# Kernel optimization log

Measured on AMD Instinct MI355X. Metric: run time of the kernel, lower is better.

Reference implementation:

```python
import jax, jax.numpy as jnp
import numpy as np

EPS = 1e-7
MIN_NORM = 1e-15
PROJ_EPS = 4e-3
C = 1.0
HEADS = 4
NEG_SLOPE = 0.2

def artanh(x):
    x = jnp.clip(x, -1.0 + EPS, 1.0 - EPS)
    return 0.5 * (jnp.log1p(x) - jnp.log1p(-x))

def _norm(x):
    return jnp.clip(jnp.linalg.norm(x, axis=-1, keepdims=True), MIN_NORM)

def proj(x, c):
    n = _norm(x)
    maxnorm = (1.0 - PROJ_EPS) / jnp.sqrt(c)
    return jnp.where(n > maxnorm, x / n * maxnorm, x)

def expmap0(u, c):
    sc = jnp.sqrt(c)
    n = _norm(u)
    return jnp.tanh(sc * n) * u / (sc * n)

def logmap0(p, c):
    sc = jnp.sqrt(c)
    n = _norm(p)
    return artanh(sc * n) * p / (sc * n)

def mobius_add(x, y, c):
    x2 = jnp.sum(x * x, -1, keepdims=True)
    y2 = jnp.sum(y * y, -1, keepdims=True)
    xy = jnp.sum(x * y, -1, keepdims=True)
    num = (1 + 2 * c * xy + c * y2) * x + (1 - c * x2) * y
    den = 1 + 2 * c * xy + c * c * x2 * y2
    return num / jnp.clip(den, MIN_NORM)

def mobius_matvec(m, x, c):
    sc = jnp.sqrt(c)
    xn = _norm(x)
    mx = x @ m.T
    mxn = _norm(mx)
    res = jnp.tanh(mxn / xn * artanh(sc * xn)) * mx / (mxn * sc)
    zero = jnp.all(mx == 0, axis=-1, keepdims=True)
    return jnp.where(zero, 0.0, res)

def segment_softmax(scores, seg, n):
    # scores: [E, H], seg: [E] destination node ids
    smax = jax.ops.segment_max(scores, seg, num_segments=n)
    smax = jnp.where(jnp.isfinite(smax), smax, 0.0)
    ex = jnp.exp(scores - smax[seg])
    den = jax.ops.segment_sum(ex, seg, num_segments=n)
    return ex / jnp.clip(den[seg], MIN_NORM)


def setup_inputs() -> dict:
    key = jax.random.key(0)
    ks = jax.random.split(key, 6)
    N, D_IN, D_OUT, E = 50000, 128, 128, 800000
    x = 0.01 * jax.random.normal(ks[0], (N, D_IN), dtype=jnp.float32)
    W = (math := np.sqrt(2.0 * 6.0 / (D_IN + D_OUT))) * jax.random.uniform(ks[1], (D_OUT, D_IN), dtype=jnp.float32, minval=-1.0, maxval=1.0)
    lin_bias = jnp.zeros((D_OUT,), jnp.float32)
    att = 0.1 * jax.random.normal(ks[2], (1, HEADS, 2 * (D_OUT // HEADS)), dtype=jnp.float32)
    conv_bias = jnp.zeros((D_OUT,), jnp.float32)
    src = jax.random.randint(ks[3], (E,), 0, N, dtype=jnp.int32)
    # guarantee no self loops (module removes them before adding canonical ones)
    dst = (src + 1 + jax.random.randint(ks[4], (E,), 0, N - 1, dtype=jnp.int32)) % N
    return {"x": x, "W": W, "lin_bias": lin_bias, "att": att,
            "conv_bias": conv_bias, "edge_src": src, "edge_dst": dst}


def reference(x, W, lin_bias, att, conv_bias, edge_src, edge_dst):
    N = x.shape[0]
    H = HEADS
    # ---- HypLinear (c=1, eval mode so no dropout) ----
    h = proj(mobius_matvec(W, x, C), C)
    hyp_bias = proj(expmap0(lin_bias, C), C)   # proj_tan0 is identity on Poincare ball
    h = proj(mobius_add(h, hyp_bias, C), C)
    D = h.shape[-1] // H
    # ---- add self loops ----
    loops = jnp.arange(N, dtype=edge_src.dtype)
    src = jnp.concatenate([edge_src, loops])   # j (source)
    dst = jnp.concatenate([edge_dst, loops])   # i (target / aggregation index)
    # ---- tangent-space GAT message passing ----
    log_x = logmap0(h, C).reshape(N, H, D)
    x_i = log_x[dst]                            # [E, H, D]
    x_j = log_x[src]                            # [E, H, D]
    att_i, att_j = att[0, :, :D], att[0, :, D:]
    alpha = jnp.einsum('ehd,hd->eh', x_i, att_i) + jnp.einsum('ehd,hd->eh', x_j, att_j)
    alpha = jax.nn.leaky_relu(alpha, NEG_SLOPE)
    alpha = segment_softmax(alpha, dst, N)      # [E, H]
    msg = x_j * alpha[:, :, None]
    out = jax.ops.segment_sum(msg, dst, num_segments=N)  # [N, H, D]
    out = out.reshape(N, H * D) + conv_bias
    # ---- update / activation / map back to manifold ----
    out = jax.nn.relu(out)                      # proj_tan0 is identity
    return proj(expmap0(out, C), C)
```

## Files before the change

kernel.cpp:

```cpp
#include <hip/hip_runtime.h>
#include <hip/hip_fp16.h>
#include <math.h>

#define EPSF 1e-7f
#define MIN_NORM 1e-15f
#define MAXNORM 0.996f
#define NEG_SLOPE 0.2f

typedef __attribute__((ext_vector_type(8))) short short8;
typedef __attribute__((ext_vector_type(4))) float f32x4;

__device__ __forceinline__ float wave_reduce_sum(float v) {
    #pragma unroll
    for (int m = 1; m < 64; m <<= 1) v += __shfl_xor(v, m, 64);
    return v;
}

__device__ __forceinline__ float artanhf_(float x) {
    x = fminf(fmaxf(x, -1.f + EPSF), 1.f - EPSF);
    return 0.5f * (log1pf(x) - log1pf(-x));
}

__device__ __forceinline__ float lrelu(float a) {
    return a < 0.f ? a * NEG_SLOPE : a;
}

__device__ __forceinline__ unsigned short f2bf(float f) {
    unsigned u = __float_as_uint(f);
    u += 0x7FFFu + ((u >> 16) & 1u);
    return (unsigned short)(u >> 16);
}
__device__ __forceinline__ float bf2f(unsigned short h) {
    return __uint_as_float(((unsigned)h) << 16);
}

__global__ void prep_kernel(const float* __restrict__ W,
                            unsigned short* __restrict__ whi,
                            unsigned short* __restrict__ wlo,
                            const float* __restrict__ lin_bias,
                            float* __restrict__ bbuf) {
    if (blockIdx.x == 64) {
        if (threadIdx.x >= 64) return;
        int lane = threadIdx.x;
        float u0 = lin_bias[lane], u1 = lin_bias[lane + 64];
        float n2 = wave_reduce_sum(u0 * u0 + u1 * u1);
        float n = fmaxf(sqrtf(n2), MIN_NORM);
        float s = tanhf(n) / n;
        float b0 = s * u0, b1 = s * u1;
        float bn = fmaxf(tanhf(n), MIN_NORM);
        float fn2 = bn * bn;
        if (bn > MAXNORM) { float f = MAXNORM / bn; b0 *= f; b1 *= f; fn2 = MAXNORM * MAXNORM; }
        bbuf[lane] = b0;
        bbuf[lane + 64] = b1;
        if (lane == 0) bbuf[128] = fn2;
        return;
    }
    int idx = blockIdx.x * 256 + threadIdx.x;
    int i = idx & 7, l = (idx >> 3) & 63, ts = idx >> 9;
    int s = ts & 3, t = ts >> 2;
    int o = t * 16 + (l & 15);
    int k = s * 32 + ((l >> 4) * 8) + i;
    float f = W[o * 128 + k];
    unsigned short h = f2bf(f);
    unsigned short lo = f2bf(f - bf2f(h));
    whi[idx] = h;
    wlo[idx] = lo;
}

#define DPAD 132
__global__ __launch_bounds__(256) void node_kernel(
    const float* __restrict__ x,
    const unsigned short* __restrict__ whi, const unsigned short* __restrict__ wlo,
    const float* __restrict__ bbuf, const float* __restrict__ att,
    unsigned short* __restrict__ log_xb,
    float* __restrict__ s_i, float* __restrict__ s_j, int N)
{
    __shared__ float mxs[16][DPAD];
    __shared__ float xn2s[16];
    int tid = threadIdx.x, wave = tid >> 6, lane = tid & 63;
    int nbase = blockIdx.x * 16;
    int arow = lane & 15, kgrp = lane >> 4;
    int anode = min(nbase + arow, N - 1);

    f32x4 acc0 = {0.f, 0.f, 0.f, 0.f};
    f32x4 acc1 = {0.f, 0.f, 0.f, 0.f};
    int t0 = wave * 2, t1 = wave * 2 + 1;
    float x2loc = 0.f;

    #pragma unroll
    for (int s = 0; s < 4; ++s) {
        const float* xp = x + (size_t)anode * 128 + s * 32 + kgrp * 8;
        float4 xa = *(const float4*)xp;
        float4 xb = *(const float4*)(xp + 4);
        float xv[8] = {xa.x, xa.y, xa.z, xa.w, xb.x, xb.y, xb.z, xb.w};
        short8 ahi, alo;
        #pragma unroll
        for (int i = 0; i < 8; ++i) {
            unsigned short h = f2bf(xv[i]);
            unsigned short l = f2bf(xv[i] - bf2f(h));
            ahi[i] = (short)h;
            alo[i] = (short)l;
        }
        if (wave == 0) {
            #pragma unroll
            for (int i = 0; i < 8; ++i) x2loc = fmaf(xv[i], xv[i], x2loc);
        }
        short8 bh0 = *(const short8*)(whi + ((size_t)(t0 * 4 + s) * 64 + lane) * 8);
        short8 bl0 = *(const short8*)(wlo + ((size_t)(t0 * 4 + s) * 64 + lane) * 8);
        short8 bh1 = *(const short8*)(whi + ((size_t)(t1 * 4 + s) * 64 + lane) * 8);
        short8 bl1 = *(const short8*)(wlo + ((size_t)(t1 * 4 + s) * 64 + lane) * 8);
        acc0 = __builtin_amdgcn_mfma_f32_16x16x32_bf16(ahi, bh0, acc0, 0, 0, 0);
        acc0 = __builtin_amdgcn_mfma_f32_16x16x32_bf16(alo, bh0, acc0, 0, 0, 0);
        acc0 = __builtin_amdgcn_mfma_f32_16x16x32_bf16(ahi, bl0, acc0, 0, 0, 0);
        acc1 = __builtin_amdgcn_mfma_f32_16x16x32_bf16(ahi, bh1, acc1, 0, 0, 0);
        acc1 = __builtin_amdgcn_mfma_f32_16x16x32_bf16(alo, bh1, acc1, 0, 0, 0);
        acc1 = __builtin_amdgcn_mfma_f32_16x16x32_bf16(ahi, bl1, acc1, 0, 0, 0);
    }
    if (wave == 0) {
        x2loc += __shfl_xor(x2loc, 16, 64);
        x2loc += __shfl_xor(x2loc, 32, 64);
        if (lane < 16) xn2s[lane] = x2loc;
    }
    #pragma unroll
    for (int r = 0; r < 4; ++r) {
        mxs[kgrp * 4 + r][t0 * 16 + arow] = acc0[r];
        mxs[kgrp * 4 + r][t1 * 16 + arow] = acc1[r];
    }
    __syncthreads();

    int g16 = lane >> 4, l16 = lane & 15;
    int nn = wave * 4 + g16;
    int node = nbase + nn;
    bool valid = node < N;
    int head = l16 >> 2;
    int dbase = l16 * 8;
    int dd8 = (l16 & 3) * 8;
    float bb[8], aiv[8], ajv[8];
    #pragma unroll
    for (int j = 0; j < 8; ++j) {
        bb[j] = bbuf[dbase + j];
        aiv[j] = att[head * 64 + dd8 + j];
        ajv[j] = att[head * 64 + 32 + dd8 + j];
    }
    float y2 = bbuf[128];

    float4 va = *(const float4*)&mxs[nn][dbase];
    float4 vb = *(const float4*)&mxs[nn][dbase + 4];
    float v[8] = {va.x, va.y, va.z, va.w, vb.x, vb.y, vb.z, vb.w};

    float mq = 0.f;
    #pragma unroll
    for (int j = 0; j < 8; ++j) mq = fmaf(v[j], v[j], mq);
    #pragma unroll
    for (int m = 1; m < 16; m <<= 1) mq += __shfl_xor(mq, m, 64);

    float xn2 = xn2s[nn];
    float xn = fmaxf(sqrtf(xn2), MIN_NORM);
    float mxn = fmaxf(sqrtf(mq), MIN_NORM);
    float t = tanhf(mxn / xn * artanhf_(xn));
    float scl = t / mxn;
    bool zero = (mq == 0.f);
    float r[8];
    #pragma unroll
    for (int j = 0; j < 8; ++j) r[j] = zero ? 0.f : scl * v[j];
    float rn2 = zero ? 0.f : t * t;
    float rn = zero ? MIN_NORM : fmaxf(fabsf(t), MIN_NORM);
    float x2 = rn2;
    if (rn > MAXNORM) {
        float f = MAXNORM / rn;
        #pragma unroll
        for (int j = 0; j < 8; ++j) r[j] *= f;
        x2 = MAXNORM * MAXNORM;
    }
    float xy = 0.f;
    #pragma unroll
    for (int j = 0; j < 8; ++j) xy = fmaf(r[j], bb[j], xy);
    #pragma unroll
    for (int m = 1; m < 16; m <<= 1) xy += __shfl_xor(xy, m, 64);
    float cA = 1.f + 2.f * xy + y2;
    float cB = 1.f - x2;
    float dn = fmaxf(1.f + 2.f * xy + x2 * y2, MIN_NORM);
    float inv = 1.f / dn;
    float h[8];
    #pragma unroll
    for (int j = 0; j < 8; ++j) h[j] = (cA * r[j] + cB * bb[j]) * inv;
    float hq = 0.f;
    #pragma unroll
    for (int j = 0; j < 8; ++j) hq = fmaf(h[j], h[j], hq);
    #pragma unroll
    for (int m = 1; m < 16; m <<= 1) hq += __shfl_xor(hq, m, 64);
    float hn = fmaxf(sqrtf(hq), MIN_NORM);
    float ln2 = hq;
    if (hn > MAXNORM) {
        float f = MAXNORM / hn;
        #pragma unroll
        for (int j = 0; j < 8; ++j) h[j] *= f;
        ln2 = MAXNORM * MAXNORM;
    }
    float lnn = fmaxf(sqrtf(ln2), MIN_NORM);
    float ls = artanhf_(lnn) / lnn;
    float lv[8];
    #pragma unroll
    for (int j = 0; j < 8; ++j) lv[j] = ls * h[j];

    if (valid) {
        uint4 pk;
        pk.x = (unsigned)f2bf(lv[0]) | ((unsigned)f2bf(lv[1]) << 16);
        pk.y = (unsigned)f2bf(lv[2]) | ((unsigned)f2bf(lv[3]) << 16);
        pk.z = (unsigned)f2bf(lv[4]) | ((unsigned)f2bf(lv[5]) << 16);
        pk.w = (unsigned)f2bf(lv[6]) | ((unsigned)f2bf(lv[7]) << 16);
        *(uint4*)&log_xb[(size_t)node * 128 + dbase] = pk;
    }
    float pi = 0.f, pj = 0.f;
    #pragma unroll
    for (int j = 0; j < 8; ++j) {
        pi = fmaf(lv[j], aiv[j], pi);
        pj = fmaf(lv[j], ajv[j], pj);
    }
    pi += __shfl_xor(pi, 1, 64); pi += __shfl_xor(pi, 2, 64);
    pj += __shfl_xor(pj, 1, 64); pj += __shfl_xor(pj, 2, 64);
    if (valid && (l16 & 3) == 0) {
        int pos = ((head & 1) << 1) | (head >> 1);
        s_i[(size_t)node * 4 + pos] = pi;
        s_j[(size_t)node * 4 + pos] = pj;
    }
}

__global__ void buildw_kernel(const int* __restrict__ src, const int* __restrict__ dst,
                              int E, const float* __restrict__ s_i,
                              const float* __restrict__ s_j,
                              int* __restrict__ head, int4* __restrict__ pair16)
{
    int e = blockIdx.x * blockDim.x + threadIdx.x;
    if (e >= E) return;
    int s_ = src[e], d_ = dst[e];
    int prev = atomicExch(&head[(size_t)d_ * 16 + (e & 15)], e);
    float4 si = *(const float4*)(s_i + (size_t)d_ * 4);
    float4 sj = *(const float4*)(s_j + (size_t)s_ * 4);
    float w0 = __expf(lrelu(si.x + sj.x));
    float w1 = __expf(lrelu(si.y + sj.y));
    float w2 = __expf(lrelu(si.z + sj.z));
    float w3 = __expf(lrelu(si.w + sj.w));
    __half2 h01 = __floats2half2_rn(w0, w1);
    __half2 h23 = __floats2half2_rn(w2, w3);
    int4 pr;
    pr.x = s_ << 8;
    pr.y = prev;
    pr.z = *(int*)&h01;
    pr.w = *(int*)&h23;
    pair16[e] = pr;
}

#define MAXS 128
__global__ __launch_bounds__(256) void aggregate_kernel(
    const int* __restrict__ head, const int4* __restrict__ pair16,
    const float* __restrict__ s_i, const float* __restrict__ s_j,
    const unsigned short* __restrict__ log_xb, const float* __restrict__ conv_bias,
    float* __restrict__ out, int N)
{
    __shared__ __align__(16) int slist[4][MAXS];
    __shared__ __align__(16) unsigned wlist[4][MAXS * 2];
    __shared__ int scnt[4];
    int tid = threadIdx.x, wave = tid >> 6, lane = tid & 63;
    int n = blockIdx.x * 4 + wave;
    bool valid = n < N;

    if (lane == 0) scnt[wave] = 0;
    __syncthreads();

    int resume = -1;
    if (valid && lane < 16) {
        int e = head[(size_t)n * 16 + lane];
        while (e >= 0) {
            int4 pr = pair16[e];
            int pos = atomicAdd(&scnt[wave], 1);
            if (pos < MAXS) {
                slist[wave][pos] = pr.x;
                wlist[wave][pos * 2]     = (unsigned)pr.z;
                wlist[wave][pos * 2 + 1] = (unsigned)pr.w;
                e = pr.y;
            } else { resume = e; break; }
        }
    }
    __syncthreads();

    int g = lane >> 5;
    float acc0 = 0.f, acc1 = 0.f, dna = 0.f, dnb = 0.f;

    int deg = 0;
    if (valid) {
        deg = min(scnt[wave], MAXS);
        float2 si2  = *(const float2*)(s_i + (size_t)n * 4 + g * 2);
        float2 sj2n = *(const float2*)(s_j + (size_t)n * 4 + g * 2);
        float ea = __expf(lrelu(si2.x + sj2n.x));
        float eb = __expf(lrelu(si2.y + sj2n.y));
        dna = ea; dnb = eb;
        const unsigned short* mrow = log_xb + (size_t)n * 128;
        acc0 = ea * bf2f(mrow[lane]);
        acc1 = eb * bf2f(mrow[lane + 64]);

        const int* sl = slist[wave];
        const unsigned* wlv = wlist[wave];
        int i = 0;
        for (; i + 4 <= deg; i += 4) {
            int4 offq = *(const int4*)&sl[i];
            int offs[4] = {offq.x, offq.y, offq.z, offq.w};
            unsigned ww[4];
            unsigned short ma[4], mb[4];
            #pragma unroll
            for (int j = 0; j < 4; ++j) {
                ww[j] = wlv[(i + j) * 2 + g];
                const unsigned short* mr =
                    (const unsigned short*)((const char*)log_xb + offs[j]);
                ma[j] = mr[lane];
                mb[j] = mr[lane + 64];
            }
            #pragma unroll
            for (int j = 0; j < 4; ++j) {
                float2 wf = __half22float2(*(const __half2*)&ww[j]);
                dna += wf.x; dnb += wf.y;
                acc0 = fmaf(wf.x, bf2f(ma[j]), acc0);
                acc1 = fmaf(wf.y, bf2f(mb[j]), acc1);
            }
        }
        for (; i < deg; ++i) {
            unsigned w = wlv[i * 2 + g];
            const unsigned short* mr =
                (const unsigned short*)((const char*)log_xb + sl[i]);
            float2 wf = __half22float2(*(const __half2*)&w);
            dna += wf.x; dnb += wf.y;
            acc0 = fmaf(wf.x, bf2f(mr[lane]), acc0);
            acc1 = fmaf(wf.y, bf2f(mr[lane + 64]), acc1);
        }
    }

    unsigned long long mask = __ballot(resume >= 0);
    while (mask) {
        int l = __ffsll((long long)mask) - 1;
        int e = __shfl(resume, l, 64);
        while (e >= 0) {
            int off = 0, nx = -1, wz = 0, wwd = 0;
            if (lane == 0) { int4 pr = pair16[e]; off = pr.x; nx = pr.y; wz = pr.z; wwd = pr.w; }
            off = __shfl(off, 0, 64);
            wz = __shfl(wz, 0, 64);
            wwd = __shfl(wwd, 0, 64);
            e = __shfl(nx, 0, 64);
            unsigned wsel = (unsigned)(g ? wwd : wz);
            float2 wf = __half22float2(*(const __half2*)&wsel);
            const unsigned short* mr = (const unsigned short*)((const char*)log_xb + off);
            dna += wf.x; dnb += wf.y;
            acc0 = fmaf(wf.x, bf2f(mr[lane]), acc0);
            acc1 = fmaf(wf.y, bf2f(mr[lane + 64]), acc1);
        }
        mask &= mask - 1;
    }

    if (!valid) return;

    float v0 = acc0 / fmaxf(dna, MIN_NORM) + conv_bias[lane];
    float v1 = acc1 / fmaxf(dnb, MIN_NORM) + conv_bias[lane + 64];
    v0 = fmaxf(v0, 0.f);
    v1 = fmaxf(v1, 0.f);
    float n2 = wave_reduce_sum(v0 * v0 + v1 * v1);
    float nn = fmaxf(sqrtf(n2), MIN_NORM);
    float tv = tanhf(nn);
    float s = tv / nn;
    float r0 = s * v0, r1 = s * v1;
    float rn = fmaxf(tv, MIN_NORM);
    if (rn > MAXNORM) { float f = MAXNORM / rn; r0 *= f; r1 *= f; }
    out[(size_t)n * 128 + lane] = r0;
    out[(size_t)n * 128 + 64 + lane] = r1;
}

extern "C" void kernel_launch(void* const* d_in, const int* in_sizes, int n_in,
                              void* d_out, int out_size, void* d_ws, size_t ws_size,
                              hipStream_t stream)
{
    const float* x        = (const float*)d_in[0];
    const float* W        = (const float*)d_in[1];
    const float* lin_bias = (const float*)d_in[2];
    const float* att      = (const float*)d_in[3];
    const float* conv_bias= (const float*)d_in[4];
    const int*   esrc     = (const int*)d_in[5];
    const int*   edst     = (const int*)d_in[6];
    int N = in_sizes[0] / 128;
    int E = in_sizes[5];
    float* out = (float*)d_out;

    char* p = (char*)d_ws;
    float* bbuf   = (float*)p;  p += 256 * 4;
    unsigned short* whi = (unsigned short*)p; p += 16384 * 2;
    unsigned short* wlo = (unsigned short*)p; p += 16384 * 2;
    float* s_i    = (float*)p;  p += (size_t)N * 4 * 4;
    float* s_j    = (float*)p;  p += (size_t)N * 4 * 4;
    int*   head   = (int*)p;    p += (size_t)N * 16 * 4;
    int4*  pair16 = (int4*)p;   p += (size_t)E * 16;
    unsigned short* log_xb = (unsigned short*)p; p += (size_t)N * 128 * 2;

    hipMemsetAsync(head, 0xFF, (size_t)N * 16 * 4, stream);

    prep_kernel<<<65, 256, 0, stream>>>(W, whi, wlo, lin_bias, bbuf);
    int nTiles = (N + 15) / 16;
    node_kernel<<<nTiles, 256, 0, stream>>>(x, whi, wlo, bbuf, att, log_xb, s_i, s_j, N);
    buildw_kernel<<<(E + 255) / 256, 256, 0, stream>>>(esrc, edst, E, s_i, s_j, head, pair16);
    aggregate_kernel<<<(N + 3) / 4, 256, 0, stream>>>(
        head, pair16, s_i, s_j, log_xb, conv_bias, out, N);
}
```

Before: 130.3 us.

## Move edge attention weight computation into aggregation and slim edge list records

The edge build kernel now stores only (src, next) pairs, 8 bytes instead of 16, and runs before the node kernel because it no longer depends on attention scores. Attention exponentials are computed per edge inside the aggregation kernel's list walk from s_i/s_j, which removes one pass over edge data but adds a random s_j gather there. The aggregation inner loop gains an 8-way unrolled path, and tanh/artanh switch to fast exp/log intrinsics, which may lose a little accuracy near the clamp boundaries.

```diff
diff --git a/kernel.cpp b/kernel.cpp
--- a/kernel.cpp
+++ b/kernel.cpp
@@ -16,9 +16,14 @@
     return v;
 }
 
-__device__ __forceinline__ float artanhf_(float x) {
+__device__ __forceinline__ float fast_tanh(float x) {
+    float e = __expf(2.f * x);
+    return 1.f - 2.f / (e + 1.f);
+}
+
+__device__ __forceinline__ float fast_artanh(float x) {
     x = fminf(fmaxf(x, -1.f + EPSF), 1.f - EPSF);
-    return 0.5f * (log1pf(x) - log1pf(-x));
+    return 0.5f * __logf((1.f + x) / (1.f - x));
 }
 
 __device__ __forceinline__ float lrelu(float a) {
@@ -157,7 +162,7 @@
     float xn2 = xn2s[nn];
     float xn = fmaxf(sqrtf(xn2), MIN_NORM);
     float mxn = fmaxf(sqrtf(mq), MIN_NORM);
-    float t = tanhf(mxn / xn * artanhf_(xn));
+    float t = fast_tanh(mxn / xn * fast_artanh(xn));
     float scl = t / mxn;
     bool zero = (mq == 0.f);
     float r[8];
@@ -198,7 +203,7 @@
         ln2 = MAXNORM * MAXNORM;
     }
     float lnn = fmaxf(sqrtf(ln2), MIN_NORM);
-    float ls = artanhf_(lnn) / lnn;
+    float ls = fast_artanh(lnn) / lnn;
     float lv[8];
     #pragma unroll
     for (int j = 0; j < 8; ++j) lv[j] = ls * h[j];
@@ -226,34 +231,19 @@
     }
 }
 
-__global__ void buildw_kernel(const int* __restrict__ src, const int* __restrict__ dst,
-                              int E, const float* __restrict__ s_i,
-                              const float* __restrict__ s_j,
-                              int* __restrict__ head, int4* __restrict__ pair16)
+__global__ void build_kernel(const int* __restrict__ src, const int* __restrict__ dst,
+                             int E, int* __restrict__ head, int2* __restrict__ pair)
 {
     int e = blockIdx.x * blockDim.x + threadIdx.x;
     if (e >= E) return;
     int s_ = src[e], d_ = dst[e];
     int prev = atomicExch(&head[(size_t)d_ * 16 + (e & 15)], e);
-    float4 si = *(const float4*)(s_i + (size_t)d_ * 4);
-    float4 sj = *(const float4*)(s_j + (size_t)s_ * 4);
-    float w0 = __expf(lrelu(si.x + sj.x));
-    float w1 = __expf(lrelu(si.y + sj.y));
-    float w2 = __expf(lrelu(si.z + sj.z));
-    float w3 = __expf(lrelu(si.w + sj.w));
-    __half2 h01 = __floats2half2_rn(w0, w1);
-    __half2 h23 = __floats2half2_rn(w2, w3);
-    int4 pr;
-    pr.x = s_ << 8;
-    pr.y = prev;
-    pr.z = *(int*)&h01;
-    pr.w = *(int*)&h23;
-    pair16[e] = pr;
+    pair[e] = make_int2(s_, prev);
 }
 
 #define MAXS 128
 __global__ __launch_bounds__(256) void aggregate_kernel(
-    const int* __restrict__ head, const int4* __restrict__ pair16,
+    const int* __restrict__ head, const int2* __restrict__ pair,
     const float* __restrict__ s_i, const float* __restrict__ s_j,
     const unsigned short* __restrict__ log_xb, const float* __restrict__ conv_bias,
     float* __restrict__ out, int N)
@@ -270,14 +260,22 @@
 
     int resume = -1;
     if (valid && lane < 16) {
+        float4 si4 = *(const float4*)(s_i + (size_t)n * 4);
         int e = head[(size_t)n * 16 + lane];
         while (e >= 0) {
-            int4 pr = pair16[e];
+            int2 pr = pair[e];
+            float4 sj4 = *(const float4*)(s_j + (size_t)pr.x * 4);
+            float w0 = __expf(lrelu(si4.x + sj4.x));
+            float w1 = __expf(lrelu(si4.y + sj4.y));
+            float w2 = __expf(lrelu(si4.z + sj4.z));
+            float w3 = __expf(lrelu(si4.w + sj4.w));
+            __half2 h01 = __floats2half2_rn(w0, w1);
+            __half2 h23 = __floats2half2_rn(w2, w3);
             int pos = atomicAdd(&scnt[wave], 1);
             if (pos < MAXS) {
-                slist[wave][pos] = pr.x;
-                wlist[wave][pos * 2]     = (unsigned)pr.z;
-                wlist[wave][pos * 2 + 1] = (unsigned)pr.w;
+                slist[wave][pos] = pr.x << 8;
+                wlist[wave][pos * 2]     = *(unsigned*)&h01;
+                wlist[wave][pos * 2 + 1] = *(unsigned*)&h23;
                 e = pr.y;
             } else { resume = e; break; }
         }
@@ -286,14 +284,16 @@
 
     int g = lane >> 5;
     float acc0 = 0.f, acc1 = 0.f, dna = 0.f, dnb = 0.f;
+    float sia = 0.f, sib = 0.f;
 
     int deg = 0;
     if (valid) {
         deg = min(scnt[wave], MAXS);
         float2 si2  = *(const float2*)(s_i + (size_t)n * 4 + g * 2);
         float2 sj2n = *(const float2*)(s_j + (size_t)n * 4 + g * 2);
-        float ea = __expf(lrelu(si2.x + sj2n.x));
-        float eb = __expf(lrelu(si2.y + sj2n.y));
+        sia = si2.x; sib = si2.y;
+        float ea = __expf(lrelu(sia + sj2n.x));
+        float eb = __expf(lrelu(sib + sj2n.y));
         dna = ea; dnb = eb;
         const unsigned short* mrow = log_xb + (size_t)n * 128;
         acc0 = ea * bf2f(mrow[lane]);
@@ -302,6 +302,29 @@
         const int* sl = slist[wave];
         const unsigned* wlv = wlist[wave];
         int i = 0;
+        for (; i + 8 <= deg; i += 8) {
+            int4 offqa = *(const int4*)&sl[i];
+            int4 offqb = *(const int4*)&sl[i + 4];
+            int offs[8] = {offqa.x, offqa.y, offqa.z, offqa.w,
+                           offqb.x, offqb.y, offqb.z, offqb.w};
+            unsigned ww[8];
+            unsigned short ma[8], mb[8];
+            #pragma unroll
+            for (int j = 0; j < 8; ++j) {
+                ww[j] = wlv[(i + j) * 2 + g];
+                const unsigned short* mr =
+                    (const unsigned short*)((const char*)log_xb + offs[j]);
+                ma[j] = mr[lane];
+                mb[j] = mr[lane + 64];
+            }
+            #pragma unroll
+            for (int j = 0; j < 8; ++j) {
+                float2 wf = __half22float2(*(const __half2*)&ww[j]);
+                dna += wf.x; dnb += wf.y;
+                acc0 = fmaf(wf.x, bf2f(ma[j]), acc0);
+                acc1 = fmaf(wf.y, bf2f(mb[j]), acc1);
+            }
+        }
         for (; i + 4 <= deg; i += 4) {
             int4 offq = *(const int4*)&sl[i];
             int offs[4] = {offq.x, offq.y, offq.z, offq.w};
@@ -339,18 +362,17 @@
         int l = __ffsll((long long)mask) - 1;
         int e = __shfl(resume, l, 64);
         while (e >= 0) {
-            int off = 0, nx = -1, wz = 0, wwd = 0;
-            if (lane == 0) { int4 pr = pair16[e]; off = pr.x; nx = pr.y; wz = pr.z; wwd = pr.w; }
-            off = __shfl(off, 0, 64);
-            wz = __shfl(wz, 0, 64);
-            wwd = __shfl(wwd, 0, 64);
+            int sv = 0, nx = -1;
+            if (lane == 0) { int2 pr = pair[e]; sv = pr.x; nx = pr.y; }
+            sv = __shfl(sv, 0, 64);
             e = __shfl(nx, 0, 64);
-            unsigned wsel = (unsigned)(g ? wwd : wz);
-            float2 wf = __half22float2(*(const __half2*)&wsel);
-            const unsigned short* mr = (const unsigned short*)((const char*)log_xb + off);
-            dna += wf.x; dnb += wf.y;
-            acc0 = fmaf(wf.x, bf2f(mr[lane]), acc0);
-            acc1 = fmaf(wf.y, bf2f(mr[lane + 64]), acc1);
+            float2 sj2 = *(const float2*)(s_j + (size_t)sv * 4 + g * 2);
+            float eA = __expf(lrelu(sia + sj2.x));
+            float eB = __expf(lrelu(sib + sj2.y));
+            const unsigned short* mr = log_xb + (size_t)sv * 128;
+            dna += eA; dnb += eB;
+            acc0 = fmaf(eA, bf2f(mr[lane]), acc0);
+            acc1 = fmaf(eB, bf2f(mr[lane + 64]), acc1);
         }
         mask &= mask - 1;
     }
@@ -363,7 +385,7 @@
     v1 = fmaxf(v1, 0.f);
     float n2 = wave_reduce_sum(v0 * v0 + v1 * v1);
     float nn = fmaxf(sqrtf(n2), MIN_NORM);
-    float tv = tanhf(nn);
+    float tv = fast_tanh(nn);
     float s = tv / nn;
     float r0 = s * v0, r1 = s * v1;
     float rn = fmaxf(tv, MIN_NORM);
@@ -394,15 +416,15 @@
     float* s_i    = (float*)p;  p += (size_t)N * 4 * 4;
     float* s_j    = (float*)p;  p += (size_t)N * 4 * 4;
     int*   head   = (int*)p;    p += (size_t)N * 16 * 4;
-    int4*  pair16 = (int4*)p;   p += (size_t)E * 16;
+    int2*  pair   = (int2*)p;   p += (size_t)E * 8;
     unsigned short* log_xb = (unsigned short*)p; p += (size_t)N * 128 * 2;
 
     hipMemsetAsync(head, 0xFF, (size_t)N * 16 * 4, stream);
 
     prep_kernel<<<65, 256, 0, stream>>>(W, whi, wlo, lin_bias, bbuf);
+    build_kernel<<<(E + 255) / 256, 256, 0, stream>>>(esrc, edst, E, head, pair);
     int nTiles = (N + 15) / 16;
     node_kernel<<<nTiles, 256, 0, stream>>>(x, whi, wlo, bbuf, att, log_xb, s_i, s_j, N);
-    buildw_kernel<<<(E + 255) / 256, 256, 0, stream>>>(esrc, edst, E, s_i, s_j, head, pair16);
     aggregate_kernel<<<(N + 3) / 4, 256, 0, stream>>>(
-        head, pair16, s_i, s_j, log_xb, conv_bias, out, N);
-}
+        head, pair, s_i, s_j, log_xb, conv_bias, out, N);
+}
```

Result: no change. 130.2 us (-0.1%).
